# Kernel optimization log

Hardware: AMD Instinct MI355X
Metric: run time of the kernel (lower is better)

## Reference

```python
import jax, jax.numpy as jnp
import numpy as np

B, N, DIM, H, DH = 2, 1024, 1024, 8, 64
DI = H * DH  # 512
K = 4        # depthwise conv kernel
EPS = 1.1920929e-07  # float32 eps (torch RMSNorm default)


def setup_inputs() -> dict:
    key = jax.random.key(0)
    ks = jax.random.split(key, 12)
    s = lambda k, shape, sc=0.02: jax.random.normal(k, shape, jnp.float32) * sc
    return dict(
        x=jax.random.normal(ks[0], (B, N, DIM), jnp.float32),
        w_rms=jnp.ones((DIM,), jnp.float32),
        wq=s(ks[1], (DIM, DI)), wk=s(ks[2], (DIM, DI)), wv=s(ks[3], (DIM, DI)),
        wo=s(ks[4], (DI, DIM)),
        conv_q=s(ks[5], (DIM, K), 0.3), conv_k=s(ks[6], (DIM, K), 0.3), conv_v=s(ks[7], (DIM, K), 0.3),
        gamma_q=jnp.ones((H, 1, DH), jnp.float32), gamma_k=jnp.ones((H, 1, DH), jnp.float32),
        lr_w=s(ks[8], (DIM, H)), lr_b=jnp.full((H,), -4.0, jnp.float32),
        decay_w=s(ks[9], (DIM, H)), decay_b=jnp.full((H,), 4.0, jnp.float32),
        mom_w=s(ks[10], (DIM, H)), mom_b=jnp.full((H,), 2.0, jnp.float32),
    )


def rmsnorm(x, w):
    return x * jax.lax.rsqrt(jnp.mean(x * x, -1, keepdims=True) + EPS) * w


def mh_rmsnorm(x, gamma):  # x: (b, h, n, d)
    rms = jnp.sqrt(jnp.sum(x * x, -1, keepdims=True)) * (DH ** -0.5)
    return x / jnp.maximum(rms, 1e-8) * gamma


def dwconv(x, w):  # x: (b, n, dim), w: (dim, K) depthwise, padding K//2 -> length n+1
    y = jax.lax.conv_general_dilated(
        x.transpose(0, 2, 1), w[:, None, :], (1,), [(K // 2, K // 2)],
        feature_group_count=DIM, dimension_numbers=('NCW', 'OIW', 'NCW'))
    return y.transpose(0, 2, 1)


def gated_scan(a, x):  # h_t = a_t h_{t-1} + x_t, h_{-1}=0; a:(bh,t), x:(bh,t,d,d)
    def combine(c1, c2):
        a1, x1 = c1
        a2, x2 = c2
        return a1 * a2, a2 * x1 + x2
    _, h = jax.lax.associative_scan(combine, (a[..., None, None], x), axis=1)
    return h


def reference(x, w_rms, wq, wk, wv, wo, conv_q, conv_k, conv_v,
              gamma_q, gamma_k, lr_w, lr_b, decay_w, decay_b, mom_w, mom_b):
    b, n, _ = x.shape
    xa = rmsnorm(x, w_rms)
    qi, ki, vi = dwconv(xa, conv_q), dwconv(xa, conv_k), dwconv(xa, conv_v)
    split = lambda t: t.reshape(b, -1, H, DH).transpose(0, 2, 1, 3)[:, :, :n]  # (b,h,n,d)
    q = mh_rmsnorm(split(qi @ wq), gamma_q)
    k = mh_rmsnorm(split(ki @ wk), gamma_k)
    v = split(vi @ wv)
    fq = q.reshape(b * H, n, DH)
    fk = k.reshape(b * H, n, DH)
    fv = v.reshape(b * H, n, DH)
    sig = jax.nn.sigmoid
    lr = sig(xa @ lr_w + lr_b).transpose(0, 2, 1).reshape(b * H, n)
    decay = sig(xa @ decay_w + decay_b).transpose(0, 2, 1).reshape(b * H, n)
    mom = sig(xa @ mom_w + mom_b).transpose(0, 2, 1).reshape(b * H, n)
    # S_ref = S0 = 0 (fresh state) => pred = 0, delta_vec = -v
    g = jnp.einsum('bti,btj->btij', -fv, fk)          # (bh, n, d, d)
    Z = gated_scan(mom, g)                             # momentum scan
    S = gated_scan(decay, -lr[..., None, None] * Z)    # memory scan
    S_prev = jnp.concatenate([jnp.zeros_like(S[:, :1]), S[:, :-1]], axis=1)
    y = jnp.einsum('btdp,btp->btd', S_prev, fq)        # retrieval y_t = S_{t-1} psi_t
    y = y.reshape(b, H, n, DH).transpose(0, 2, 1, 3).reshape(b, n, DI)
    return y @ wo
```

## Files before the change

### kernel.cpp

```cpp
#include <hip/hip_runtime.h>
#include <math.h>

#define DEV __device__ __forceinline__

constexpr int Bb   = 2;
constexpr int Seq  = 1024;
constexpr int Dim  = 1024;
constexpr int Hh   = 8;
constexpr int Dh   = 64;
constexpr int Di   = 512;
constexpr int BN   = Bb * Seq;
constexpr int NSEQ = Bb * Hh;
constexpr int CHUNK = 32;
constexpr int CLEN  = Seq / CHUNK;
constexpr float EPSV = 1.1920929e-07f;
constexpr int NT2  = 8;
constexpr int KSPL = 8;

typedef _Float16 half8 __attribute__((ext_vector_type(8)));
typedef float    f32x4 __attribute__((ext_vector_type(4)));

DEV float bf2f(unsigned short u) {
  union { unsigned int i; float f; } x; x.i = ((unsigned int)u) << 16; return x.f;
}
DEV unsigned short f2bf(float f) {
  union { float f; unsigned int i; } x; x.f = f;
  unsigned int r = x.i + 0x7fffu + ((x.i >> 16) & 1u);
  return (unsigned short)(r >> 16);
}
DEV float ldin(const void* p, int f32, size_t i) {
  if (f32) return ((const float*)p)[i];
  return bf2f(((const unsigned short*)p)[i]);
}
DEV void ld4(const void* p, int f32, size_t i, float* dst) {
  if (f32) {
    float4 u = *(const float4*)((const float*)p + i);
    dst[0] = u.x; dst[1] = u.y; dst[2] = u.z; dst[3] = u.w;
  } else {
    ushort4 u = *(const ushort4*)((const unsigned short*)p + i);
    dst[0] = bf2f(u.x); dst[1] = bf2f(u.y); dst[2] = bf2f(u.z); dst[3] = bf2f(u.w);
  }
}
DEV int sniff_vote(const void* p, int n, int tid) {
  int j = 2 * tid, valid = 0, bad = 0;
  if (j < n) {
    valid = 1;
    float v = bf2f(((const unsigned short*)p)[j]);
    float a = fabsf(v);
    if (!(a >= 1e-12f && a <= 1e4f)) bad = 1;
  }
#pragma unroll
  for (int m = 1; m < 64; m <<= 1) { valid += __shfl_xor(valid, m); bad += __shfl_xor(bad, m); }
  return (2 * bad > valid) ? 1 : 0;
}

struct InPtrs { const void* p[17]; int n[17]; };

__global__ __launch_bounds__(256) void k_prep_all(
    InPtrs ip,
    int* __restrict__ flags,
    _Float16* __restrict__ wqT, _Float16* __restrict__ wkT,
    _Float16* __restrict__ wvT, _Float16* __restrict__ woT,
    _Float16* __restrict__ WgT,
    _Float16* __restrict__ wcq, _Float16* __restrict__ wck,
    _Float16* __restrict__ wcv,
    float* __restrict__ gqf, float* __restrict__ gkf, float* __restrict__ gbf)
{
  int blk = blockIdx.x;
  int tid = threadIdx.x;
  __shared__ int sfl[8];

  if (blk < 1024) {
    int z = blk >> 8, bx = blk & 15, by = (blk >> 4) & 15;
    int idx = (z == 0) ? 2 : ((z == 1) ? 3 : ((z == 2) ? 4 : 5));
    const void* src = ip.p[idx];
    _Float16* dst   = (z == 0) ? wqT : ((z == 1) ? wkT : ((z == 2) ? wvT : woT));
    int Kd = (z < 3) ? Dim : Di;
    int Nn = (z < 3) ? Di : Dim;
    int n0 = bx * 64, k0 = by * 64;
    if (n0 >= Nn || k0 >= Kd) return;

    if (tid < 64) { int f = sniff_vote(src, ip.n[idx], tid); if (tid == 0) sfl[0] = f; }
    __syncthreads();
    int f = sfl[0];

    __shared__ float tile[64][65];
    int r = tid >> 4, c4 = (tid & 15) * 4;
#pragma unroll
    for (int rr = 0; rr < 4; ++rr) {
      int k = rr * 16 + r;
      ld4(src, f, (size_t)(k0 + k) * Nn + n0 + c4, &tile[k][c4]);
    }
    __syncthreads();
#pragma unroll
    for (int rr = 0; rr < 4; ++rr) {
      int n = rr * 16 + r;
      _Float16 o4[4];
#pragma unroll
      for (int j = 0; j < 4; ++j) o4[j] = (_Float16)tile[c4 + j][n];
      *(ushort4*)&dst[(size_t)(n0 + n) * Kd + k0 + c4] = *(ushort4*)o4;
    }
  } else if (blk < 1088) {
    int row = blk - 1024;
    if (row < 24) {
      int g = row >> 3, h = row & 7;
      int idx = (g == 0) ? 11 : ((g == 1) ? 13 : 15);
      const void* W = ip.p[idx];
      if (tid < 64) { int f = sniff_vote(W, ip.n[idx], tid); if (tid == 0) sfl[0] = f; }
      __syncthreads();
      int f = sfl[0];
#pragma unroll
      for (int it = 0; it < 4; ++it) {
        int d = it * 256 + tid;
        WgT[(size_t)row * Dim + d] = (_Float16)ldin(W, f, (size_t)d * Hh + h);
      }
    } else {
#pragma unroll
      for (int it = 0; it < 4; ++it)
        WgT[(size_t)row * Dim + it * 256 + tid] = (_Float16)0.f;
    }
  } else if (blk < 1104) {
    if (tid < 64) {
      int f6 = sniff_vote(ip.p[6], ip.n[6], tid);
      int f7 = sniff_vote(ip.p[7], ip.n[7], tid);
      int f8 = sniff_vote(ip.p[8], ip.n[8], tid);
      if (tid == 0) { sfl[0] = f6; sfl[1] = f7; sfl[2] = f8; }
    }
    __syncthreads();
    int e = (blk - 1088) * 256 + tid;
    wcq[e] = (_Float16)ldin(ip.p[6], sfl[0], e);
    wck[e] = (_Float16)ldin(ip.p[7], sfl[1], e);
    wcv[e] = (_Float16)ldin(ip.p[8], sfl[2], e);
  } else {
    __shared__ int allf[17];
    for (int ii = 0; ii < 17; ++ii) {
      if (tid < 64) {
        int f = sniff_vote(ip.p[ii], ip.n[ii], tid);
        if (tid == 0) { flags[ii] = f; allf[ii] = f; }
      }
    }
    __syncthreads();
    int f9 = allf[9], f10 = allf[10];
    for (int i = tid; i < Di; i += 256) {
      gqf[i] = ldin(ip.p[9], f9, i);
      gkf[i] = ldin(ip.p[10], f10, i);
    }
    if (tid < 24) {
      int g = tid >> 3, h = tid & 7;
      int idx = (g == 0) ? 12 : ((g == 1) ? 14 : 16);
      gbf[tid] = ldin(ip.p[idx], allf[idx], h);
    }
  }
}

__global__ __launch_bounds__(256) void k_rmsconv(
    const void* __restrict__ x, const void* __restrict__ w_rms,
    const int* __restrict__ flags,
    const _Float16* __restrict__ wcq, const _Float16* __restrict__ wck,
    const _Float16* __restrict__ wcv,
    _Float16* __restrict__ xaf,
    _Float16* __restrict__ qc, _Float16* __restrict__ kc,
    _Float16* __restrict__ vc)
{
  constexpr int NR = NT2 + 3;
  __shared__ _Float16 xas[NR][Dim];
  int tb = blockIdx.x, b = blockIdx.y;
  int t0 = tb * NT2;
  int tid = threadIdx.x, lane = tid & 63, wv = tid >> 6;
  int fx = flags[0], fw = flags[1];
  int e0 = lane * 16;

  float wr[16];
#pragma unroll
  for (int q = 0; q < 4; ++q) ld4(w_rms, fw, e0 + q * 4, &wr[q * 4]);

  for (int rr = wv; rr < NR; rr += 4) {
    int r = t0 - 2 + rr;
    float xv[16];
    bool inr = (r >= 0 && r < Seq);
    if (inr) {
      size_t rb = (size_t)(b * Seq + r) * Dim + e0;
#pragma unroll
      for (int q = 0; q < 4; ++q) ld4(x, fx, rb + q * 4, &xv[q * 4]);
    } else {
#pragma unroll
      for (int j = 0; j < 16; ++j) xv[j] = 0.f;
    }
    float ss = 0.f;
#pragma unroll
    for (int j = 0; j < 16; ++j) ss = fmaf(xv[j], xv[j], ss);
#pragma unroll
    for (int m = 1; m < 64; m <<= 1) ss += __shfl_xor(ss, m);
    float scale = rsqrtf(ss * (1.0f / Dim) + EPSV);

    _Float16 o[16];
#pragma unroll
    for (int j = 0; j < 16; ++j) o[j] = (_Float16)(xv[j] * scale * wr[j]);
    *(uint4*)&xas[rr][e0]     = *(uint4*)&o[0];
    *(uint4*)&xas[rr][e0 + 8] = *(uint4*)&o[8];
    if (inr && r >= t0 && r < t0 + NT2) {
      size_t ob = (size_t)(b * Seq + r) * Dim + e0;
      *(uint4*)&xaf[ob]     = *(uint4*)&o[0];
      *(uint4*)&xaf[ob + 8] = *(uint4*)&o[8];
    }
  }
  __syncthreads();

  int c0 = tid * 4;
  _Float16 lwq[16], lwk[16], lwv[16];
  *(uint4*)&lwq[0] = *(const uint4*)&wcq[c0 * 4];
  *(uint4*)&lwq[8] = *(const uint4*)&wcq[c0 * 4 + 8];
  *(uint4*)&lwk[0] = *(const uint4*)&wck[c0 * 4];
  *(uint4*)&lwk[8] = *(const uint4*)&wck[c0 * 4 + 8];
  *(uint4*)&lwv[0] = *(const uint4*)&wcv[c0 * 4];
  *(uint4*)&lwv[8] = *(const uint4*)&wcv[c0 * 4 + 8];

#pragma unroll
  for (int tt = 0; tt < NT2; ++tt) {
    float rv[4][4];
#pragma unroll
    for (int k = 0; k < 4; ++k) {
      _Float16 hx[4];
      *(ushort4*)hx = *(const ushort4*)&xas[tt + k][c0];
#pragma unroll
      for (int j = 0; j < 4; ++j) rv[k][j] = (float)hx[j];
    }
    _Float16 tq[4], tk[4], tv[4];
#pragma unroll
    for (int j = 0; j < 4; ++j) {
      float aq = rv[0][j] * (float)lwq[j * 4 + 0] + rv[1][j] * (float)lwq[j * 4 + 1]
               + rv[2][j] * (float)lwq[j * 4 + 2] + rv[3][j] * (float)lwq[j * 4 + 3];
      float ak = rv[0][j] * (float)lwk[j * 4 + 0] + rv[1][j] * (float)lwk[j * 4 + 1]
               + rv[2][j] * (float)lwk[j * 4 + 2] + rv[3][j] * (float)lwk[j * 4 + 3];
      float av = rv[0][j] * (float)lwv[j * 4 + 0] + rv[1][j] * (float)lwv[j * 4 + 1]
               + rv[2][j] * (float)lwv[j * 4 + 2] + rv[3][j] * (float)lwv[j * 4 + 3];
      tq[j] = (_Float16)aq; tk[j] = (_Float16)ak; tv[j] = (_Float16)av;
    }
    size_t o = ((size_t)(b * Seq + t0 + tt)) * Dim + c0;
    *(ushort4*)&qc[o] = *(ushort4*)tq;
    *(ushort4*)&kc[o] = *(ushort4*)tk;
    *(ushort4*)&vc[o] = *(ushort4*)tv;
  }
}

__global__ __launch_bounds__(256) void k_mid(
    const _Float16* __restrict__ qc, const _Float16* __restrict__ kc,
    const _Float16* __restrict__ vc,
    const _Float16* __restrict__ wqT, const _Float16* __restrict__ wkT,
    const _Float16* __restrict__ wvT,
    const _Float16* __restrict__ xaf, const _Float16* __restrict__ WgT,
    _Float16* __restrict__ qpre, _Float16* __restrict__ kpre,
    _Float16* __restrict__ vpre,
    float* __restrict__ gpart)
{
  __shared__ __align__(16) _Float16 As[128][40];
  __shared__ __align__(16) _Float16 Bs[64][40];

  int blk = blockIdx.x;
  int tid = threadIdx.x, lane = tid & 63, wv = tid >> 6;
  int mrow = lane & 15, quad = lane >> 4;

  if (blk < 384) {
    int z = blk / 128, rem = blk - z * 128;
    int by = rem >> 3, bx = rem & 7;
    const _Float16* A  = (z == 0) ? qc : ((z == 1) ? kc : vc);
    const _Float16* Bt = (z == 0) ? wqT : ((z == 1) ? wkT : wvT);
    _Float16* C        = (z == 0) ? qpre : ((z == 1) ? kpre : vpre);
    int n0 = bx * 64, m0 = by * 128;
    int wm = wv * 32;
    int ar0 = tid >> 2, ac0 = (tid & 3) * 8;
    int ar1 = (tid + 256) >> 2;

    f32x4 acc[2][4];
#pragma unroll
    for (int mi = 0; mi < 2; ++mi)
#pragma unroll
      for (int ni = 0; ni < 4; ++ni) acc[mi][ni] = (f32x4){0.f, 0.f, 0.f, 0.f};

    for (int kt = 0; kt < Dim; kt += 32) {
      __syncthreads();
      *(uint4*)&As[ar0][ac0] = *(const uint4*)&A[(size_t)(m0 + ar0) * Dim + kt + ac0];
      *(uint4*)&As[ar1][ac0] = *(const uint4*)&A[(size_t)(m0 + ar1) * Dim + kt + ac0];
      *(uint4*)&Bs[ar0][ac0] = *(const uint4*)&Bt[(size_t)(n0 + ar0) * Dim + kt + ac0];
      __syncthreads();

      half8 bfr[4];
#pragma unroll
      for (int ni = 0; ni < 4; ++ni)
        bfr[ni] = *(const half8*)&Bs[ni * 16 + mrow][quad * 8];
#pragma unroll
      for (int mi = 0; mi < 2; ++mi) {
        half8 afr = *(const half8*)&As[wm + mi * 16 + mrow][quad * 8];
#pragma unroll
        for (int ni = 0; ni < 4; ++ni)
          acc[mi][ni] = __builtin_amdgcn_mfma_f32_16x16x32_f16(afr, bfr[ni], acc[mi][ni], 0, 0, 0);
      }
    }

#pragma unroll
    for (int mi = 0; mi < 2; ++mi) {
#pragma unroll
      for (int ni = 0; ni < 4; ++ni) {
        int col = n0 + ni * 16 + mrow;
#pragma unroll
        for (int r2 = 0; r2 < 4; ++r2) {
          int row = m0 + wm + mi * 16 + quad * 4 + r2;
          C[(size_t)row * Di + col] = (_Float16)acc[mi][ni][r2];
        }
      }
    }
  } else {
    int g = blk - 384;
    int m0 = (g & 31) * 64, ks = g >> 5;
    int srow = tid >> 2, scol = (tid & 3) * 8;
    int kbase = ks * (Dim / KSPL);

    f32x4 acc[4];
#pragma unroll
    for (int mi = 0; mi < 4; ++mi) acc[mi] = (f32x4){0.f, 0.f, 0.f, 0.f};

    for (int kt = kbase; kt < kbase + Dim / KSPL; kt += 32) {
      __syncthreads();
      *(uint4*)&As[srow][scol] = *(const uint4*)&xaf[(size_t)(m0 + srow) * Dim + kt + scol];
      *(uint4*)&Bs[srow][scol] = *(const uint4*)&WgT[(size_t)srow * Dim + kt + scol];
      __syncthreads();
      half8 bfr = *(const half8*)&Bs[wv * 16 + mrow][quad * 8];
#pragma unroll
      for (int mi = 0; mi < 4; ++mi) {
        half8 afr = *(const half8*)&As[mi * 16 + mrow][quad * 8];
        acc[mi] = __builtin_amdgcn_mfma_f32_16x16x32_f16(afr, bfr, acc[mi], 0, 0, 0);
      }
    }

    int col = wv * 16 + mrow;
    if (col < 24) {
#pragma unroll
      for (int mi = 0; mi < 4; ++mi) {
#pragma unroll
        for (int r2 = 0; r2 < 4; ++r2) {
          int row = m0 + mi * 16 + quad * 4 + r2;
          gpart[((size_t)ks * BN + row) * 32 + col] = acc[mi][r2];
        }
      }
    }
  }
}

__global__ __launch_bounds__(256) void k_gemm_fin(
    const _Float16* __restrict__ A, const _Float16* __restrict__ Bt,
    void* __restrict__ C, const int* __restrict__ flags, int Nn, int Kd)
{
  __shared__ __align__(16) _Float16 As[128][40];
  __shared__ __align__(16) _Float16 Bs[64][40];

  int tid = threadIdx.x, lane = tid & 63, wv = tid >> 6;
  int n0 = blockIdx.x * 64, m0 = blockIdx.y * 128;
  int mrow = lane & 15, quad = lane >> 4;
  int wm = wv * 32;
  int ar0 = tid >> 2, ac0 = (tid & 3) * 8;
  int ar1 = (tid + 256) >> 2;

  f32x4 acc[2][4];
#pragma unroll
  for (int mi = 0; mi < 2; ++mi)
#pragma unroll
    for (int ni = 0; ni < 4; ++ni) acc[mi][ni] = (f32x4){0.f, 0.f, 0.f, 0.f};

  for (int kt = 0; kt < Kd; kt += 32) {
    __syncthreads();
    *(uint4*)&As[ar0][ac0] = *(const uint4*)&A[(size_t)(m0 + ar0) * Kd + kt + ac0];
    *(uint4*)&As[ar1][ac0] = *(const uint4*)&A[(size_t)(m0 + ar1) * Kd + kt + ac0];
    *(uint4*)&Bs[ar0][ac0] = *(const uint4*)&Bt[(size_t)(n0 + ar0) * Kd + kt + ac0];
    __syncthreads();

    half8 bfr[4];
#pragma unroll
    for (int ni = 0; ni < 4; ++ni)
      bfr[ni] = *(const half8*)&Bs[ni * 16 + mrow][quad * 8];
#pragma unroll
    for (int mi = 0; mi < 2; ++mi) {
      half8 afr = *(const half8*)&As[wm + mi * 16 + mrow][quad * 8];
#pragma unroll
      for (int ni = 0; ni < 4; ++ni)
        acc[mi][ni] = __builtin_amdgcn_mfma_f32_16x16x32_f16(afr, bfr[ni], acc[mi][ni], 0, 0, 0);
    }
  }

  int any_bf16 = 0;
#pragma unroll
  for (int i2 = 0; i2 < 17; ++i2) any_bf16 |= (flags[i2] == 0);

#pragma unroll
  for (int mi = 0; mi < 2; ++mi) {
#pragma unroll
    for (int ni = 0; ni < 4; ++ni) {
      int col = n0 + ni * 16 + mrow;
#pragma unroll
      for (int r2 = 0; r2 < 4; ++r2) {
        int row = m0 + wm + mi * 16 + quad * 4 + r2;
        float v = acc[mi][ni][r2];
        size_t idx = (size_t)row * Nn + col;
        if (any_bf16) ((unsigned short*)C)[idx] = f2bf(v);
        else          ((float*)C)[idx] = v;
      }
    }
  }
}

DEV void load_gates(const float* __restrict__ gpart, const float* __restrict__ gbf,
                    int b, int h, int c, int tid,
                    float* gl, float* gd, float* gm)
{
  if (tid < 96) {
    int which = tid >> 5, t2 = tid & 31;
    int col = which * 8 + h;
    int row = b * Seq + c * CLEN + t2;
    float acc = gbf[col];
#pragma unroll
    for (int ks = 0; ks < KSPL; ++ks)
      acc += gpart[((size_t)ks * BN + row) * 32 + col];
    float sg = 1.f / (1.f + expf(-acc));
    if (which == 0) gl[t2] = sg; else if (which == 1) gd[t2] = sg; else gm[t2] = sg;
  }
}

__global__ __launch_bounds__(256) void k_phaseA(
    const _Float16* __restrict__ kpre, const _Float16* __restrict__ vpre,
    const float* __restrict__ gkf,
    const float* __restrict__ gpart, const float* __restrict__ gbf,
    _Float16* __restrict__ ZS_Z, _Float16* __restrict__ ZS_S,
    float* __restrict__ Mc, float* __restrict__ Dc, float* __restrict__ Wc)
{
  int c = blockIdx.x, s = blockIdx.y;
  int b = s >> 3, h = s & 7;
  int tid = threadIdx.x, lane = tid & 63, wv = tid >> 6;
  int i = tid >> 2, j0 = (tid & 3) * 16;
  __shared__ float kn[CLEN][64], vv[CLEN][64];
  __shared__ float gl[CLEN], gd[CLEN], gm[CLEN];

  {
    int t = tid >> 3, col = (tid & 7) * 8;
    size_t g = ((size_t)(b * Seq + c * CLEN + t)) * Di + h * 64 + col;
    half8 kv = *(const half8*)&kpre[g];
    half8 vvv = *(const half8*)&vpre[g];
#pragma unroll
    for (int j = 0; j < 8; ++j) { kn[t][col + j] = (float)kv[j]; vv[t][col + j] = (float)vvv[j]; }
    load_gates(gpart, gbf, b, h, c, tid, gl, gd, gm);
  }
  __syncthreads();
  {
    float gk = gkf[h * 64 + lane];
#pragma unroll
    for (int tt = 0; tt < 8; ++tt) {
      int t = wv * 8 + tt;
      float kvv = kn[t][lane];
      float ss = kvv * kvv;
#pragma unroll
      for (int m = 1; m < 64; m <<= 1) ss += __shfl_xor(ss, m);
      kn[t][lane] = kvv * (1.f / fmaxf(sqrtf(ss) * 0.125f, 1e-8f)) * gk;
    }
  }
  __syncthreads();

  float Zl[16], Sl[16];
#pragma unroll
  for (int jj = 0; jj < 16; ++jj) { Zl[jj] = 0.f; Sl[jj] = 0.f; }
  float Mcum = 1.f, Dcum = 1.f, wacc = 0.f;

  for (int t = 0; t < CLEN; ++t) {
    float l = gl[t], dd = gd[t], mm = gm[t];
    float vi = vv[t][i];
    Mcum *= mm;
#pragma unroll
    for (int jj = 0; jj < 16; ++jj) {
      Zl[jj] = fmaf(mm, Zl[jj], -vi * kn[t][j0 + jj]);
      Sl[jj] = fmaf(dd, Sl[jj], -l * Zl[jj]);
    }
    wacc = fmaf(dd, wacc, -l * Mcum);
    Dcum *= dd;
  }
  size_t base = ((size_t)(s * CHUNK + c)) * 4096 + (size_t)i * 64 + j0;
  half8 zo0, zo1, so0, so1;
#pragma unroll
  for (int jj = 0; jj < 8; ++jj) {
    zo0[jj] = (_Float16)Zl[jj];     zo1[jj] = (_Float16)Zl[jj + 8];
    so0[jj] = (_Float16)Sl[jj];     so1[jj] = (_Float16)Sl[jj + 8];
  }
  *(half8*)&ZS_Z[base] = zo0; *(half8*)&ZS_Z[base + 8] = zo1;
  *(half8*)&ZS_S[base] = so0; *(half8*)&ZS_S[base + 8] = so1;
  if (tid == 0) {
    Mc[s * CHUNK + c] = Mcum; Dc[s * CHUNK + c] = Dcum; Wc[s * CHUNK + c] = wacc;
  }
}

__global__ __launch_bounds__(256) void k_phaseB(
    _Float16* __restrict__ ZS_Z, _Float16* __restrict__ ZS_S,
    const float* __restrict__ Mc, const float* __restrict__ Dc,
    const float* __restrict__ Wc)
{
  int s = blockIdx.x;
  int e = blockIdx.y * 256 + threadIdx.x;
  float Z = 0.f, S = 0.f;
  for (int c = 0; c < CHUNK; ++c) {
    size_t base = ((size_t)(s * CHUNK + c)) * 4096 + e;
    float mc = Mc[s * CHUNK + c], dc = Dc[s * CHUNK + c], wc = Wc[s * CHUNK + c];
    float zl = (float)ZS_Z[base], sl = (float)ZS_S[base];
    ZS_Z[base] = (_Float16)Z; ZS_S[base] = (_Float16)S;
    S = fmaf(dc, S, fmaf(wc, Z, sl));
    Z = fmaf(mc, Z, zl);
  }
}

__global__ __launch_bounds__(256) void k_phaseC(
    const _Float16* __restrict__ qpre, const _Float16* __restrict__ kpre,
    const _Float16* __restrict__ vpre,
    const float* __restrict__ gqf, const float* __restrict__ gkf,
    const float* __restrict__ gpart, const float* __restrict__ gbf,
    const _Float16* __restrict__ ZS_Z, const _Float16* __restrict__ ZS_S,
    _Float16* __restrict__ yb)
{
  int c = blockIdx.x, s = blockIdx.y;
  int b = s >> 3, h = s & 7;
  int tid = threadIdx.x, lane = tid & 63, wv = tid >> 6;
  int i = tid >> 2, j0 = (tid & 3) * 16;
  __shared__ float kn[CLEN][64], vv[CLEN][64], qn[CLEN][64];
  __shared__ float gl[CLEN], gd[CLEN], gm[CLEN];

  float Zi_[16], Si_[16], Zl[16], Sl[16];
  size_t base = ((size_t)(s * CHUNK + c)) * 4096 + (size_t)i * 64 + j0;
  {
    half8 z0 = *(const half8*)&ZS_Z[base], z1 = *(const half8*)&ZS_Z[base + 8];
    half8 s0 = *(const half8*)&ZS_S[base], s1 = *(const half8*)&ZS_S[base + 8];
#pragma unroll
    for (int jj = 0; jj < 8; ++jj) {
      Zi_[jj] = (float)z0[jj]; Zi_[jj + 8] = (float)z1[jj];
      Si_[jj] = (float)s0[jj]; Si_[jj + 8] = (float)s1[jj];
      Zl[jj] = 0.f; Zl[jj + 8] = 0.f; Sl[jj] = 0.f; Sl[jj + 8] = 0.f;
    }
  }
  {
    int t = tid >> 3, col = (tid & 7) * 8;
    size_t g = ((size_t)(b * Seq + c * CLEN + t)) * Di + h * 64 + col;
    half8 kv = *(const half8*)&kpre[g];
    half8 vvv = *(const half8*)&vpre[g];
    half8 qv = *(const half8*)&qpre[g];
#pragma unroll
    for (int j = 0; j < 8; ++j) {
      kn[t][col + j] = (float)kv[j]; vv[t][col + j] = (float)vvv[j];
      qn[t][col + j] = (float)qv[j];
    }
    load_gates(gpart, gbf, b, h, c, tid, gl, gd, gm);
  }
  __syncthreads();
  {
    float gk = gkf[h * 64 + lane];
    float gq = gqf[h * 64 + lane];
#pragma unroll
    for (int tt = 0; tt < 8; ++tt) {
      int t = wv * 8 + tt;
      float kvv = kn[t][lane];
      float ssk = kvv * kvv;
      float qvv = qn[t][lane];
      float ssq = qvv * qvv;
#pragma unroll
      for (int m = 1; m < 64; m <<= 1) { ssk += __shfl_xor(ssk, m); ssq += __shfl_xor(ssq, m); }
      kn[t][lane] = kvv * (1.f / fmaxf(sqrtf(ssk) * 0.125f, 1e-8f)) * gk;
      qn[t][lane] = qvv * (1.f / fmaxf(sqrtf(ssq) * 0.125f, 1e-8f)) * gq;
    }
  }
  __syncthreads();

  float Mcum = 1.f, Dcum = 1.f, wacc = 0.f;
  float Dprev = 1.f, wprev = 0.f;

  for (int t = 0; t < CLEN; ++t) {
    float l = gl[t], dd = gd[t], mm = gm[t];

    float yp = 0.f;
#pragma unroll
    for (int jj = 0; jj < 16; ++jj) {
      float tmp = fmaf(Dprev, Si_[jj], fmaf(wprev, Zi_[jj], Sl[jj]));
      yp = fmaf(tmp, qn[t][j0 + jj], yp);
    }
    yp += __shfl_xor(yp, 1);
    yp += __shfl_xor(yp, 2);
    if ((tid & 3) == 0)
      yb[((size_t)(b * Seq + c * CLEN + t)) * Di + h * 64 + i] = (_Float16)yp;

    float vi = vv[t][i];
    Mcum *= mm;
#pragma unroll
    for (int jj = 0; jj < 16; ++jj) {
      Zl[jj] = fmaf(mm, Zl[jj], -vi * kn[t][j0 + jj]);
      Sl[jj] = fmaf(dd, Sl[jj], -l * Zl[jj]);
    }
    wacc = fmaf(dd, wacc, -l * Mcum);
    Dcum *= dd;
    Dprev = Dcum; wprev = wacc;
  }
}

extern "C" void kernel_launch(void* const* d_in, const int* in_sizes, int n_in,
                              void* d_out, int out_size, void* d_ws, size_t ws_size,
                              hipStream_t stream) {
  InPtrs ip;
  for (int i = 0; i < 17; ++i) { ip.p[i] = d_in[i]; ip.n[i] = in_sizes[i]; }

  char* p = (char*)d_ws;
  auto take = [&](size_t bytes) -> char* {
    char* q = p; p += (bytes + 255) & ~(size_t)255; return q;
  };
  int* flags           = (int*)take(32 * 4);
  _Float16* xaf        = (_Float16*)take((size_t)BN * Dim * 2);
  _Float16* qc         = (_Float16*)take((size_t)BN * Dim * 2);
  _Float16* kc         = (_Float16*)take((size_t)BN * Dim * 2);
  _Float16* vc         = (_Float16*)take((size_t)BN * Dim * 2);
  _Float16* qpre       = (_Float16*)take((size_t)BN * Di * 2);
  _Float16* kpre       = (_Float16*)take((size_t)BN * Di * 2);
  _Float16* vpre       = (_Float16*)take((size_t)BN * Di * 2);
  float* gpart         = (float*)take((size_t)KSPL * BN * 32 * 4);
  float* Mc            = (float*)take((size_t)NSEQ * CHUNK * 4);
  float* Dc            = (float*)take((size_t)NSEQ * CHUNK * 4);
  float* Wc            = (float*)take((size_t)NSEQ * CHUNK * 4);
  _Float16* wqT        = (_Float16*)take((size_t)Di * Dim * 2);
  _Float16* wkT        = (_Float16*)take((size_t)Di * Dim * 2);
  _Float16* wvT        = (_Float16*)take((size_t)Di * Dim * 2);
  _Float16* woT        = (_Float16*)take((size_t)Dim * Di * 2);
  _Float16* WgT        = (_Float16*)take((size_t)64 * Dim * 2);
  _Float16* wcq        = (_Float16*)take((size_t)Dim * 4 * 2);
  _Float16* wck        = (_Float16*)take((size_t)Dim * 4 * 2);
  _Float16* wcv        = (_Float16*)take((size_t)Dim * 4 * 2);
  float* gqf           = (float*)take(Di * 4);
  float* gkf           = (float*)take(Di * 4);
  float* gbf           = (float*)take(32 * 4);
  _Float16* ZS_Z       = qc;
  _Float16* ZS_S       = kc;
  _Float16* yb         = vc;

  k_prep_all<<<1105, 256, 0, stream>>>(ip, flags, wqT, wkT, wvT, woT, WgT,
                                       wcq, wck, wcv, gqf, gkf, gbf);

  k_rmsconv<<<dim3(Seq / NT2, Bb), 256, 0, stream>>>(
      d_in[0], d_in[1], flags, wcq, wck, wcv, xaf, qc, kc, vc);

  k_mid<<<640, 256, 0, stream>>>(qc, kc, vc, wqT, wkT, wvT, xaf, WgT,
                                 qpre, kpre, vpre, gpart);

  k_phaseA<<<dim3(CHUNK, NSEQ), 256, 0, stream>>>(kpre, vpre, gkf,
                                                  gpart, gbf,
                                                  ZS_Z, ZS_S, Mc, Dc, Wc);
  k_phaseB<<<dim3(NSEQ, 16), 256, 0, stream>>>(ZS_Z, ZS_S, Mc, Dc, Wc);
  k_phaseC<<<dim3(CHUNK, NSEQ), 256, 0, stream>>>(qpre, kpre, vpre, gqf, gkf,
                                                  gpart, gbf,
                                                  ZS_Z, ZS_S, yb);

  k_gemm_fin<<<dim3(Dim / 64, BN / 128), 256, 0, stream>>>(
      yb, woT, d_out, flags, Dim, Di);
}
```

Baseline: 187.4 us.

## Use direct global-to-LDS loads and larger 128x128 tiles in QKV and output GEMMs

Replaces register-staged global-to-shared copies with the global_load_lds builtin, which writes 16-byte chunks straight into unpadded LDS tiles, in both the QKV projection and the final output GEMM. The QKV GEMM tile grows from 128x64 to 128x128, with each wave computing a 64x64 sub-tile, so more MFMA work is done per LDS load and fewer blocks are launched (448 instead of 640). The removed LDS padding may bring bank conflicts on fragment reads. The larger accumulator arrays raise register pressure, and fewer blocks may leave compute units underused.

Measured after the change: 184.8 us. About the same (-1.4%).

```diff
diff --git a/kernel.cpp b/kernel.cpp
--- a/kernel.cpp
+++ b/kernel.cpp
@@ -54,6 +54,12 @@
   return (2 * bad > valid) ? 1 : 0;
 }
 
+DEV void gld16(const _Float16* g, _Float16* l) {
+  __builtin_amdgcn_global_load_lds(
+      (const __attribute__((address_space(1))) void*)g,
+      (__attribute__((address_space(3))) void*)l, 16, 0, 0);
+}
+
 struct InPtrs { const void* p[17]; int n[17]; };
 
 __global__ __launch_bounds__(256) void k_prep_all(
@@ -253,64 +259,71 @@
     _Float16* __restrict__ vpre,
     float* __restrict__ gpart)
 {
-  __shared__ __align__(16) _Float16 As[128][40];
-  __shared__ __align__(16) _Float16 Bs[64][40];
+  __shared__ __align__(16) _Float16 ldsbuf[256 * 32];
 
   int blk = blockIdx.x;
   int tid = threadIdx.x, lane = tid & 63, wv = tid >> 6;
   int mrow = lane & 15, quad = lane >> 4;
 
-  if (blk < 384) {
-    int z = blk / 128, rem = blk - z * 128;
-    int by = rem >> 3, bx = rem & 7;
+  if (blk < 192) {
+    int z = blk >> 6, rem = blk & 63;
+    int by = rem >> 2, bx = rem & 3;
     const _Float16* A  = (z == 0) ? qc : ((z == 1) ? kc : vc);
     const _Float16* Bt = (z == 0) ? wqT : ((z == 1) ? wkT : wvT);
     _Float16* C        = (z == 0) ? qpre : ((z == 1) ? kpre : vpre);
-    int n0 = bx * 64, m0 = by * 128;
-    int wm = wv * 32;
-    int ar0 = tid >> 2, ac0 = (tid & 3) * 8;
-    int ar1 = (tid + 256) >> 2;
-
-    f32x4 acc[2][4];
-#pragma unroll
-    for (int mi = 0; mi < 2; ++mi)
+    int m0 = by * 128, n0 = bx * 128;
+    int wr = wv >> 1, wc = wv & 1;
+
+    _Float16* Asl = ldsbuf;
+    _Float16* Bsl = ldsbuf + 128 * 32;
+
+    int sr = lane >> 2, sc = (lane & 3) * 8;
+
+    f32x4 acc[4][4];
+#pragma unroll
+    for (int mi = 0; mi < 4; ++mi)
 #pragma unroll
       for (int ni = 0; ni < 4; ++ni) acc[mi][ni] = (f32x4){0.f, 0.f, 0.f, 0.f};
 
     for (int kt = 0; kt < Dim; kt += 32) {
       __syncthreads();
-      *(uint4*)&As[ar0][ac0] = *(const uint4*)&A[(size_t)(m0 + ar0) * Dim + kt + ac0];
-      *(uint4*)&As[ar1][ac0] = *(const uint4*)&A[(size_t)(m0 + ar1) * Dim + kt + ac0];
-      *(uint4*)&Bs[ar0][ac0] = *(const uint4*)&Bt[(size_t)(n0 + ar0) * Dim + kt + ac0];
+      gld16(&A [(size_t)(m0 + wv * 32      + sr) * Dim + kt + sc], &Asl[(wv * 32     ) * 32]);
+      gld16(&A [(size_t)(m0 + wv * 32 + 16 + sr) * Dim + kt + sc], &Asl[(wv * 32 + 16) * 32]);
+      gld16(&Bt[(size_t)(n0 + wv * 32      + sr) * Dim + kt + sc], &Bsl[(wv * 32     ) * 32]);
+      gld16(&Bt[(size_t)(n0 + wv * 32 + 16 + sr) * Dim + kt + sc], &Bsl[(wv * 32 + 16) * 32]);
       __syncthreads();
 
-      half8 bfr[4];
-#pragma unroll
-      for (int ni = 0; ni < 4; ++ni)
-        bfr[ni] = *(const half8*)&Bs[ni * 16 + mrow][quad * 8];
-#pragma unroll
-      for (int mi = 0; mi < 2; ++mi) {
-        half8 afr = *(const half8*)&As[wm + mi * 16 + mrow][quad * 8];
+      half8 afr[4], bfr[4];
+#pragma unroll
+      for (int i = 0; i < 4; ++i)
+        afr[i] = *(const half8*)&Asl[(wr * 64 + i * 16 + mrow) * 32 + quad * 8];
+#pragma unroll
+      for (int i = 0; i < 4; ++i)
+        bfr[i] = *(const half8*)&Bsl[(wc * 64 + i * 16 + mrow) * 32 + quad * 8];
+#pragma unroll
+      for (int mi = 0; mi < 4; ++mi)
 #pragma unroll
         for (int ni = 0; ni < 4; ++ni)
-          acc[mi][ni] = __builtin_amdgcn_mfma_f32_16x16x32_f16(afr, bfr[ni], acc[mi][ni], 0, 0, 0);
-      }
-    }
-
-#pragma unroll
-    for (int mi = 0; mi < 2; ++mi) {
+          acc[mi][ni] = __builtin_amdgcn_mfma_f32_16x16x32_f16(afr[mi], bfr[ni], acc[mi][ni], 0, 0, 0);
+    }
+
+#pragma unroll
+    for (int mi = 0; mi < 4; ++mi) {
 #pragma unroll
       for (int ni = 0; ni < 4; ++ni) {
-        int col = n0 + ni * 16 + mrow;
+        int col = n0 + wc * 64 + ni * 16 + mrow;
 #pragma unroll
         for (int r2 = 0; r2 < 4; ++r2) {
-          int row = m0 + wm + mi * 16 + quad * 4 + r2;
+          int row = m0 + wr * 64 + mi * 16 + quad * 4 + r2;
           C[(size_t)row * Di + col] = (_Float16)acc[mi][ni][r2];
         }
       }
     }
   } else {
-    int g = blk - 384;
+    _Float16 (*As)[40] = (_Float16(*)[40])ldsbuf;
+    _Float16 (*Bs)[40] = (_Float16(*)[40])(ldsbuf + 128 * 40);
+
+    int g = blk - 192;
     int m0 = (g & 31) * 64, ks = g >> 5;
     int srow = tid >> 2, scol = (tid & 3) * 8;
     int kbase = ks * (Dim / KSPL);
@@ -350,15 +363,15 @@
     const _Float16* __restrict__ A, const _Float16* __restrict__ Bt,
     void* __restrict__ C, const int* __restrict__ flags, int Nn, int Kd)
 {
-  __shared__ __align__(16) _Float16 As[128][40];
-  __shared__ __align__(16) _Float16 Bs[64][40];
+  __shared__ __align__(16) _Float16 lds[(128 + 64) * 32];
+  _Float16* Asl = lds;
+  _Float16* Bsl = lds + 128 * 32;
 
   int tid = threadIdx.x, lane = tid & 63, wv = tid >> 6;
   int n0 = blockIdx.x * 64, m0 = blockIdx.y * 128;
   int mrow = lane & 15, quad = lane >> 4;
   int wm = wv * 32;
-  int ar0 = tid >> 2, ac0 = (tid & 3) * 8;
-  int ar1 = (tid + 256) >> 2;
+  int sr = lane >> 2, sc = (lane & 3) * 8;
 
   f32x4 acc[2][4];
 #pragma unroll
@@ -368,18 +381,18 @@
 
   for (int kt = 0; kt < Kd; kt += 32) {
     __syncthreads();
-    *(uint4*)&As[ar0][ac0] = *(const uint4*)&A[(size_t)(m0 + ar0) * Kd + kt + ac0];
-    *(uint4*)&As[ar1][ac0] = *(const uint4*)&A[(size_t)(m0 + ar1) * Kd + kt + ac0];
-    *(uint4*)&Bs[ar0][ac0] = *(const uint4*)&Bt[(size_t)(n0 + ar0) * Kd + kt + ac0];
+    gld16(&A [(size_t)(m0 + wv * 32      + sr) * Kd + kt + sc], &Asl[(wv * 32     ) * 32]);
+    gld16(&A [(size_t)(m0 + wv * 32 + 16 + sr) * Kd + kt + sc], &Asl[(wv * 32 + 16) * 32]);
+    gld16(&Bt[(size_t)(n0 + wv * 16      + sr) * Kd + kt + sc], &Bsl[(wv * 16     ) * 32]);
     __syncthreads();
 
     half8 bfr[4];
 #pragma unroll
     for (int ni = 0; ni < 4; ++ni)
-      bfr[ni] = *(const half8*)&Bs[ni * 16 + mrow][quad * 8];
+      bfr[ni] = *(const half8*)&Bsl[(ni * 16 + mrow) * 32 + quad * 8];
 #pragma unroll
     for (int mi = 0; mi < 2; ++mi) {
-      half8 afr = *(const half8*)&As[wm + mi * 16 + mrow][quad * 8];
+      half8 afr = *(const half8*)&Asl[(wm + mi * 16 + mrow) * 32 + quad * 8];
 #pragma unroll
       for (int ni = 0; ni < 4; ++ni)
         acc[mi][ni] = __builtin_amdgcn_mfma_f32_16x16x32_f16(afr, bfr[ni], acc[mi][ni], 0, 0, 0);
@@ -643,7 +656,7 @@
   k_rmsconv<<<dim3(Seq / NT2, Bb), 256, 0, stream>>>(
       d_in[0], d_in[1], flags, wcq, wck, wcv, xaf, qc, kc, vc);
 
-  k_mid<<<640, 256, 0, stream>>>(qc, kc, vc, wqT, wkT, wvT, xaf, WgT,
+  k_mid<<<448, 256, 0, stream>>>(qc, kc, vc, wqT, wkT, wvT, xaf, WgT,
                                  qpre, kpre, vpre, gpart);
 
   k_phaseA<<<dim3(CHUNK, NSEQ), 256, 0, stream>>>(kpre, vpre, gkf,
```
